# Kernel optimization log

Hardware: AMD Instinct MI355X
Metric: run time of the kernel (lower is better)

## Reference

```python
import jax, jax.numpy as jnp
import numpy as np

L, H, FG, C = 2, 4, 8, 2            # n_layer, grid_heads, grid_feats, grid_channels
HNODE, HNET, HPIN = 96, 32, 16      # hidden node/net/pin feats
ONODE, ONET, NT = 32, 32, 4         # out node/net feats, n_target


def _leaky(x, s=0.01):
    return jnp.where(x >= 0, x, s * x)


def _edge_softmax(e, dst, n):
    # e: [E,H] scores, softmax over incoming edges per dst node
    m = jax.ops.segment_max(e, dst, num_segments=n)
    m = jnp.where(jnp.isfinite(m), m, 0.0)
    ex = jnp.exp(e - m[dst])
    s = jax.ops.segment_sum(ex, dst, num_segments=n)
    return ex / jnp.maximum(s[dst], 1e-9)


def _gat(x, src, dst, fc_w, attn_l, attn_r, bias, n):
    # DGL GATConv: fc (no bias), additive attention, leaky_relu(0.2), edge softmax, sum, +bias
    h = (x @ fc_w).reshape(n, H, FG)                      # [N,H,F]
    el = jnp.sum(h * attn_l, -1)                          # [N,H]
    er = jnp.sum(h * attn_r, -1)
    e = _leaky(el[src] + er[dst], 0.2)                    # [E,H]
    a = _edge_softmax(e, dst, n)
    out = jax.ops.segment_sum(h[src] * a[..., None], dst, num_segments=n)
    return out + bias.reshape(1, H, FG)                   # [N,H,F]


def _graphconv(x, src, dst, w, b, n_src, n_dst):
    # DGL GraphConv norm='both': D_src^-1/2 (xW) aggregated, D_dst^-1/2, + bias
    deg_out = jnp.maximum(jax.ops.segment_sum(jnp.ones(src.shape, jnp.float32), src, num_segments=n_src), 1.0)
    deg_in = jnp.maximum(jax.ops.segment_sum(jnp.ones(dst.shape, jnp.float32), dst, num_segments=n_dst), 1.0)
    h = (x * deg_out[:, None] ** -0.5) @ w
    agg = jax.ops.segment_sum(h[src], dst, num_segments=n_dst)
    return agg * deg_in[:, None] ** -0.5 + b


def _nnconv(x_src, src, dst, efeat, lin2_w, lin2_b, b, n_dst):
    # DGL NNConv (aggregator='mean'): per-edge weight matrix from edge_func=lin2
    W = (efeat @ lin2_w + lin2_b).reshape(-1, HNET, ONODE)   # [E,in,out]
    msg = jnp.einsum('ei,eio->eo', x_src[src], W)            # [E,out]
    deg = jnp.maximum(jax.ops.segment_sum(jnp.ones(dst.shape, jnp.float32), dst, num_segments=n_dst), 1.0)
    agg = jax.ops.segment_sum(msg, dst, num_segments=n_dst) / deg[:, None]
    return agg + b


def setup_inputs() -> dict:
    key = jax.random.key(0)
    ks = jax.random.split(key, 32)
    Nn, Nnet, Ep, Eg = 50000, 50000, 150000, 400000
    IN_NODE, IN_NET, IN_PIN = 16, 8, 8

    def rn(k, shape, scale=0.1):
        return jax.random.normal(k, shape, jnp.float32) * scale

    return {
        'in_node_feat': rn(ks[0], (Nn, IN_NODE), 1.0),
        'in_net_feat': rn(ks[1], (Nnet, IN_NET), 1.0),
        'in_pin_feat': rn(ks[2], (Ep, IN_PIN), 1.0),
        'node_lin_w': rn(ks[3], (IN_NODE, HNODE)), 'node_lin_b': rn(ks[4], (HNODE,)),
        'net_lin_w': rn(ks[5], (IN_NET, HNET)), 'net_lin_b': rn(ks[6], (HNET,)),
        'pin_lin_w': rn(ks[7], (IN_PIN, HPIN)), 'pin_lin_b': rn(ks[8], (HPIN,)),
        'gat_fc_w': rn(ks[9], (L, HNODE, H * FG)),
        'gat_attn_l': rn(ks[10], (L, H, FG)), 'gat_attn_r': rn(ks[11], (L, H, FG)),
        'gat_bias': rn(ks[12], (L, H * FG)),
        'gconv_w': rn(ks[13], (L, HNODE, ONET)), 'gconv_b': rn(ks[14], (L, ONET)),
        'lin2_w': rn(ks[15], (L, HPIN, HNET * ONODE)), 'lin2_b': rn(ks[16], (L, HNET * ONODE)),
        'nnconv_b': rn(ks[17], (L, ONODE)),
        'out1_w': rn(ks[18], (IN_NODE + HNODE, HNODE)), 'out1_b': rn(ks[19], (HNODE,)),
        'out2_w': rn(ks[20], (HNODE, HNODE)), 'out2_b': rn(ks[21], (HNODE,)),
        'out3_w': rn(ks[22], (HNODE, NT)), 'out3_b': rn(ks[23], (NT,)),
        'pins_src': jax.random.randint(ks[24], (Ep,), 0, Nn),
        'pins_dst': jax.random.randint(ks[25], (Ep,), 0, Nnet),
        'grid_src': jax.random.randint(ks[26], (C, Eg), 0, Nn),
        'grid_dst': jax.random.randint(ks[27], (C, Eg), 0, Nn),
    }


def reference(in_node_feat, in_net_feat, in_pin_feat, node_lin_w, node_lin_b,
              net_lin_w, net_lin_b, pin_lin_w, pin_lin_b, gat_fc_w, gat_attn_l,
              gat_attn_r, gat_bias, gconv_w, gconv_b, lin2_w, lin2_b, nnconv_b,
              out1_w, out1_b, out2_w, out2_b, out3_w, out3_b,
              pins_src, pins_dst, grid_src, grid_dst):
    Nn = in_node_feat.shape[0]
    Nnet = in_net_feat.shape[0]
    node = _leaky(in_node_feat @ node_lin_w + node_lin_b)
    net = _leaky(in_net_feat @ net_lin_w + net_lin_b)
    pin = _leaky(in_pin_feat @ pin_lin_w + pin_lin_b)
    for i in range(L):
        grids = [_gat(node, grid_src[j], grid_dst[j], gat_fc_w[i], gat_attn_l[i],
                      gat_attn_r[i], gat_bias[i], Nn) for j in range(C)]
        grid_out = jnp.concatenate(grids, -1).reshape(Nn, -1)   # [N, H*C*FG]
        # 'pins': node -> net (GraphConv); 'pinned': net -> node (NNConv, reversed pin edges)
        net_out = _graphconv(node, pins_src, pins_dst, gconv_w[i], gconv_b[i], Nn, Nnet)
        node_out = _nnconv(net, pins_dst, pins_src, pin, lin2_w[i], lin2_b[i], nnconv_b[i], Nn)
        node = jnp.tanh(jnp.concatenate([grid_out, node_out], -1))
        net = jnp.tanh(net_out)
    h = jnp.tanh(jnp.concatenate([in_node_feat, node], -1) @ out1_w + out1_b)
    h = jnp.tanh(h @ out2_w + out2_b)
    return jax.nn.sigmoid(h @ out3_w + out3_b)
```

## Files before the change

### kernel.cpp

```cpp
#include <hip/hip_runtime.h>
#include <math.h>


#define CAPG 48
#define CAPP 24
#define GB_U16 64
#define PD_U16 32
#define PS_STRIDE 64

typedef unsigned short ushort_t;
typedef unsigned int uint_t;
static __device__ __forceinline__ float bf2f(ushort_t u) {
    return __uint_as_float(((unsigned)u) << 16);
}
static __device__ __forceinline__ ushort_t f2bf(float f) {
    unsigned i = __float_as_uint(f);
    unsigned r = (i + 0x7FFFu + ((i >> 16) & 1u)) >> 16;
    return (ushort_t)r;
}
static __device__ __forceinline__ uint_t pk2(float a, float b) {
    return (uint_t)f2bf(a) | ((uint_t)f2bf(b) << 16);
}
static __device__ __forceinline__ float lo2(uint_t u) { return __uint_as_float(u << 16); }
static __device__ __forceinline__ float hi2(uint_t u) { return __uint_as_float(u & 0xFFFF0000u); }

template <int ACT, int K1, int K2, int M, int R, bool OUT16>
__global__ void gemm_tiled(const float* __restrict__ X1,
                           const float* __restrict__ X2,
                           const float* __restrict__ rowscale,
                           const float* __restrict__ W,
                           const float* __restrict__ bias,
                           void* __restrict__ Yv, int N) {
    constexpr int K = K1 + K2;
    constexpr int MG = M / 4;
    constexpr int RG = 256 / MG;
    __shared__ float sW[K * M];
    for (int t = threadIdx.x; t < K * M; t += 256) sW[t] = W[t];
    __syncthreads();
    const float4* sW4 = (const float4*)sW;
    const int lane = threadIdx.x % MG;
    const int rsub = threadIdx.x / MG;
    if (rsub >= RG) return;
    const long long bstride = (long long)gridDim.x * RG * R;
    for (long long base = (long long)blockIdx.x * RG * R + rsub; base < N; base += bstride) {
        long long rows[R];
        bool ok[R];
        float4 acc[R];
#pragma unroll
        for (int j = 0; j < R; ++j) {
            rows[j] = base + (long long)j * RG;
            ok[j] = rows[j] < N;
            if (!ok[j]) rows[j] = base;
            acc[j] = {0.f, 0.f, 0.f, 0.f};
        }
        {
            const float4* x4[R];
#pragma unroll
            for (int j = 0; j < R; ++j) x4[j] = (const float4*)(X1 + rows[j] * K1);
#pragma unroll 2
            for (int k4 = 0; k4 < K1 / 4; ++k4) {
                float4 w0 = sW4[(k4 * 4 + 0) * MG + lane];
                float4 w1 = sW4[(k4 * 4 + 1) * MG + lane];
                float4 w2 = sW4[(k4 * 4 + 2) * MG + lane];
                float4 w3 = sW4[(k4 * 4 + 3) * MG + lane];
#pragma unroll
                for (int j = 0; j < R; ++j) {
                    float4 xv = x4[j][k4];
                    acc[j].x += xv.x * w0.x + xv.y * w1.x + xv.z * w2.x + xv.w * w3.x;
                    acc[j].y += xv.x * w0.y + xv.y * w1.y + xv.z * w2.y + xv.w * w3.y;
                    acc[j].z += xv.x * w0.z + xv.y * w1.z + xv.z * w2.z + xv.w * w3.z;
                    acc[j].w += xv.x * w0.w + xv.y * w1.w + xv.z * w2.w + xv.w * w3.w;
                }
            }
        }
        if (K2 > 0) {
            const float4* x4[R];
#pragma unroll
            for (int j = 0; j < R; ++j) x4[j] = (const float4*)(X2 + rows[j] * K2);
#pragma unroll 2
            for (int k4 = 0; k4 < K2 / 4; ++k4) {
                float4 w0 = sW4[(K1 + k4 * 4 + 0) * MG + lane];
                float4 w1 = sW4[(K1 + k4 * 4 + 1) * MG + lane];
                float4 w2 = sW4[(K1 + k4 * 4 + 2) * MG + lane];
                float4 w3 = sW4[(K1 + k4 * 4 + 3) * MG + lane];
#pragma unroll
                for (int j = 0; j < R; ++j) {
                    float4 xv = x4[j][k4];
                    acc[j].x += xv.x * w0.x + xv.y * w1.x + xv.z * w2.x + xv.w * w3.x;
                    acc[j].y += xv.x * w0.y + xv.y * w1.y + xv.z * w2.y + xv.w * w3.y;
                    acc[j].z += xv.x * w0.z + xv.y * w1.z + xv.z * w2.z + xv.w * w3.z;
                    acc[j].w += xv.x * w0.w + xv.y * w1.w + xv.z * w2.w + xv.w * w3.w;
                }
            }
        }
#pragma unroll
        for (int j = 0; j < R; ++j) {
            if (!ok[j]) continue;
            float4 a = acc[j];
            if (rowscale) {
                float rs = rowscale[rows[j]];
                a.x *= rs; a.y *= rs; a.z *= rs; a.w *= rs;
            }
            if (bias) {
                float4 bv = *(const float4*)(bias + lane * 4);
                a.x += bv.x; a.y += bv.y; a.z += bv.z; a.w += bv.w;
            }
            if (ACT == 1) {
                a.x = a.x >= 0.f ? a.x : 0.01f * a.x;
                a.y = a.y >= 0.f ? a.y : 0.01f * a.y;
                a.z = a.z >= 0.f ? a.z : 0.01f * a.z;
                a.w = a.w >= 0.f ? a.w : 0.01f * a.w;
            } else if (ACT == 2) {
                a.x = tanhf(a.x); a.y = tanhf(a.y);
                a.z = tanhf(a.z); a.w = tanhf(a.w);
            } else if (ACT == 3) {
                a.x = 1.f / (1.f + expf(-a.x)); a.y = 1.f / (1.f + expf(-a.y));
                a.z = 1.f / (1.f + expf(-a.z)); a.w = 1.f / (1.f + expf(-a.w));
            }
            if (OUT16) {
                uint2 v;
                v.x = pk2(a.x, a.y);
                v.y = pk2(a.z, a.w);
                *(uint2*)((ushort_t*)Yv + rows[j] * M + lane * 4) = v;
            } else {
                *(float4*)((float*)Yv + rows[j] * M + lane * 4) = a;
            }
        }
    }
}

__global__ void gemm_dual32(const float* __restrict__ X,
                            const float* __restrict__ rsN,
                            const float* __restrict__ W1,
                            const float* __restrict__ W2,
                            ushort_t* __restrict__ Y1, ushort_t* __restrict__ Y2, int N) {
    __shared__ float sW1[96 * 32];
    __shared__ float sW2[96 * 32];
    for (int t = threadIdx.x; t < 96 * 32; t += 256) {
        sW1[t] = W1[t];
        sW2[t] = W2[t];
    }
    __syncthreads();
    const float4* sW1_4 = (const float4*)sW1;
    const float4* sW2_4 = (const float4*)sW2;
    const int lane = threadIdx.x & 7;
    const int rsub = threadIdx.x >> 3;
    long long n0 = (long long)blockIdx.x * 64 + rsub;
    long long n1 = n0 + 32;
    if (n0 >= N) return;
    bool ok1 = n1 < N;
    const float4* x0 = (const float4*)(X + n0 * 96);
    const float4* x1 = (const float4*)(X + (ok1 ? n1 : n0) * 96);
    float4 a0 = {0.f, 0.f, 0.f, 0.f}, b0 = a0, a1 = a0, b1 = a0;
#pragma unroll 2
    for (int k4 = 0; k4 < 24; ++k4) {
        float4 xv0 = x0[k4];
        float4 xv1 = x1[k4];
#pragma unroll
        for (int kk = 0; kk < 4; ++kk) {
            float4 w1v = sW1_4[(k4 * 4 + kk) * 8 + lane];
            float4 w2v = sW2_4[(k4 * 4 + kk) * 8 + lane];
            float xs0 = kk == 0 ? xv0.x : kk == 1 ? xv0.y : kk == 2 ? xv0.z : xv0.w;
            float xs1 = kk == 0 ? xv1.x : kk == 1 ? xv1.y : kk == 2 ? xv1.z : xv1.w;
            a0.x += xs0 * w1v.x; a0.y += xs0 * w1v.y; a0.z += xs0 * w1v.z; a0.w += xs0 * w1v.w;
            b0.x += xs0 * w2v.x; b0.y += xs0 * w2v.y; b0.z += xs0 * w2v.z; b0.w += xs0 * w2v.w;
            a1.x += xs1 * w1v.x; a1.y += xs1 * w1v.y; a1.z += xs1 * w1v.z; a1.w += xs1 * w1v.w;
            b1.x += xs1 * w2v.x; b1.y += xs1 * w2v.y; b1.z += xs1 * w2v.z; b1.w += xs1 * w2v.w;
        }
    }
    {
        float rs = rsN[n0];
        uint2 va = {pk2(a0.x, a0.y), pk2(a0.z, a0.w)};
        uint2 vb = {pk2(b0.x * rs, b0.y * rs), pk2(b0.z * rs, b0.w * rs)};
        *(uint2*)(Y1 + n0 * 32 + lane * 4) = va;
        *(uint2*)(Y2 + n0 * 32 + lane * 4) = vb;
    }
    if (ok1) {
        float rs = rsN[n1];
        uint2 va = {pk2(a1.x, a1.y), pk2(a1.z, a1.w)};
        uint2 vb = {pk2(b1.x * rs, b1.y * rs), pk2(b1.z * rs, b1.w * rs)};
        *(uint2*)(Y1 + n1 * 32 + lane * 4) = va;
        *(uint2*)(Y2 + n1 * 32 + lane * 4) = vb;
    }
}

__global__ void zero_counts(ushort_t* __restrict__ gB0, ushort_t* __restrict__ gB1,
                            ushort_t* __restrict__ pdB, int* __restrict__ psB,
                            int Nn, int Nnet) {
    int i = blockIdx.x * blockDim.x + threadIdx.x;
    int mx = Nn > Nnet ? Nn : Nnet;
    for (; i < mx; i += gridDim.x * blockDim.x) {
        if (i < Nn) {
            *(int*)(gB0 + (long long)i * GB_U16) = 0;
            *(int*)(gB1 + (long long)i * GB_U16) = 0;
            psB[(long long)i * PS_STRIDE] = 0;
        }
        if (i < Nnet) *(int*)(pdB + (long long)i * PD_U16) = 0;
    }
}

__global__ void csr_build(const int* __restrict__ ps, const int* __restrict__ pd,
                          const int* __restrict__ gs0, const int* __restrict__ gd0,
                          const int* __restrict__ gs1, const int* __restrict__ gd1,
                          ushort_t* __restrict__ gB0, ushort_t* __restrict__ gB1,
                          ushort_t* __restrict__ pdB, int* __restrict__ psB,
                          int Ep, int Eg) {
    int total = 2 * Ep + 2 * Eg;
    for (int t = blockIdx.x * blockDim.x + threadIdx.x; t < total; t += gridDim.x * blockDim.x) {
        if (t < Ep) {
            int s = ps[t];
            int* b = psB + (long long)s * PS_STRIDE;
            int r = atomicAdd(b, 1);
            if (r < CAPP) ((int2*)b)[1 + r] = make_int2(t, pd[t]);
        } else if (t < 2 * Ep) {
            int e = t - Ep;
            int d = pd[e];
            ushort_t* b = pdB + (long long)d * PD_U16;
            int r = atomicAdd((int*)b, 1);
            if (r < CAPP) b[2 + r] = (ushort_t)ps[e];
        } else if (t < 2 * Ep + Eg) {
            int e = t - 2 * Ep;
            int d = gd0[e];
            ushort_t* b = gB0 + (long long)d * GB_U16;
            int r = atomicAdd((int*)b, 1);
            if (r < CAPG) b[2 + r] = (ushort_t)gs0[e];
        } else {
            int e = t - 2 * Ep - Eg;
            int d = gd1[e];
            ushort_t* b = gB1 + (long long)d * GB_U16;
            int r = atomicAdd((int*)b, 1);
            if (r < CAPG) b[2 + r] = (ushort_t)gs1[e];
        }
    }
}

__global__ void deg_xform2(const int* __restrict__ psB, const ushort_t* __restrict__ pdB,
                           float* __restrict__ rs, float* __restrict__ inv,
                           float* __restrict__ rsNet, int Nn, int Nnet) {
    int i = blockIdx.x * blockDim.x + threadIdx.x;
    int mx = Nn > Nnet ? Nn : Nnet;
    for (; i < mx; i += gridDim.x * blockDim.x) {
        if (i < Nn) {
            float d = fmaxf((float)psB[(long long)i * PS_STRIDE], 1.f);
            rs[i] = 1.f / sqrtf(d);
            inv[i] = 1.f / d;
        }
        if (i < Nnet) {
            float d = fmaxf((float)*(const int*)(pdB + (long long)i * PD_U16), 1.f);
            rsNet[i] = 1.f / sqrtf(d);
        }
    }
}

__global__ void gat_scores(const ushort_t* __restrict__ h, const float* __restrict__ al,
                           const float* __restrict__ ar, float* __restrict__ el,
                           float* __restrict__ er, int N) {
    int idx = blockIdx.x * blockDim.x + threadIdx.x;
    if (idx >= N * 4) return;
    int n = idx >> 2, hd = idx & 3;
    uint4 hv = *(const uint4*)(h + (long long)n * 32 + hd * 8);
    float f0 = lo2(hv.x), f1 = hi2(hv.x), f2 = lo2(hv.y), f3 = hi2(hv.y);
    float f4 = lo2(hv.z), f5 = hi2(hv.z), f6 = lo2(hv.w), f7 = hi2(hv.w);
    const float* a = al + hd * 8;
    const float* r = ar + hd * 8;
    float sl = f0 * a[0] + f1 * a[1] + f2 * a[2] + f3 * a[3] +
               f4 * a[4] + f5 * a[5] + f6 * a[6] + f7 * a[7];
    float sr = f0 * r[0] + f1 * r[1] + f2 * r[2] + f3 * r[3] +
               f4 * r[4] + f5 * r[5] + f6 * r[6] + f7 * r[7];
    el[idx] = sl;
    er[idx] = sr;
}

__global__ void gat_gather8(const ushort_t* __restrict__ gB0, const ushort_t* __restrict__ gB1,
                            const float* __restrict__ el, const float* __restrict__ er,
                            const ushort_t* __restrict__ gh, const float* __restrict__ gbias,
                            float* __restrict__ out, int N) {
    int idx = blockIdx.x * blockDim.x + threadIdx.x;
    if (idx >= N * 8) return;
    int d = idx >> 3;
    int rem = idx & 7;
    int hd = rem >> 1;
    int ch = rem & 1;
    float rd = er[d * 4 + hd];
    const ushort_t* b = (ch ? gB1 : gB0) + (long long)d * GB_U16;
    int c = *(const int*)b;
    c = c < CAPG ? c : CAPG;
    float sum = 0.f;
    float acc0 = 0.f, acc1 = 0.f, acc2 = 0.f, acc3 = 0.f;
    float acc4 = 0.f, acc5 = 0.f, acc6 = 0.f, acc7 = 0.f;
    for (int p = 0; p < c; ++p) {
        int s = b[2 + p];
        float v = el[s * 4 + hd] + rd;
        v = v >= 0.f ? v : 0.2f * v;
        float w = __expf(v);
        uint4 hv = *(const uint4*)(gh + (long long)s * 32 + hd * 8);
        sum += w;
        acc0 += w * lo2(hv.x); acc1 += w * hi2(hv.x);
        acc2 += w * lo2(hv.y); acc3 += w * hi2(hv.y);
        acc4 += w * lo2(hv.z); acc5 += w * hi2(hv.z);
        acc6 += w * lo2(hv.w); acc7 += w * hi2(hv.w);
    }
    float inv = 1.f / fmaxf(sum, 1e-9f);
    const float4* gb4 = (const float4*)(gbias + hd * 8);
    float4 b0 = gb4[0], b1 = gb4[1];
    float* op = out + (long long)d * 96 + hd * 16 + ch * 8;
    float4 r0, r1;
    r0.x = tanhf(acc0 * inv + b0.x); r0.y = tanhf(acc1 * inv + b0.y);
    r0.z = tanhf(acc2 * inv + b0.z); r0.w = tanhf(acc3 * inv + b0.w);
    r1.x = tanhf(acc4 * inv + b1.x); r1.y = tanhf(acc5 * inv + b1.y);
    r1.z = tanhf(acc6 * inv + b1.z); r1.w = tanhf(acc7 * inv + b1.w);
    *(float4*)(op) = r0;
    *(float4*)(op + 4) = r1;
}

__global__ void gconv_gather(const ushort_t* __restrict__ pdB, const ushort_t* __restrict__ h,
                             const float* __restrict__ rsNet, const float* __restrict__ gb,
                             ushort_t* __restrict__ out, int N) {
    long long total = (long long)N * 32;
    long long stride = (long long)gridDim.x * blockDim.x;
    for (long long idx = (long long)blockIdx.x * blockDim.x + threadIdx.x; idx < total; idx += stride) {
        int n = (int)(idx >> 5), c = (int)(idx & 31);
        const ushort_t* b = pdB + (long long)n * PD_U16;
        int cn = *(const int*)b;
        cn = cn < CAPP ? cn : CAPP;
        float acc = 0.f;
        for (int p = 0; p < cn; ++p) acc += bf2f(h[(long long)b[2 + p] * 32 + c]);
        out[idx] = f2bf(tanhf(acc * rsNet[n] + gb[c]));
    }
}

__global__ void nn_accum(const int* __restrict__ psB, const float* __restrict__ pinf,
                         const ushort_t* __restrict__ net, ushort_t* __restrict__ G, int N) {
    int t = blockIdx.x * blockDim.x + threadIdx.x;
    int n = t >> 5, i = t & 31;
    if (n >= N) return;
    const int* b = psB + (long long)n * PS_STRIDE;
    int cn = b[0]; cn = cn < CAPP ? cn : CAPP;
    const int2* ed2 = (const int2*)b + 1;
    float g[17];
#pragma unroll
    for (int k = 0; k < 17; ++k) g[k] = 0.f;
    for (int p = 0; p < cn; ++p) {
        int2 ed = ed2[p];
        float nv = bf2f(net[(long long)ed.y * 32 + i]);
        const float4* pr4 = (const float4*)(pinf + (long long)ed.x * 16);
        float4 a0 = pr4[0], a1 = pr4[1], a2 = pr4[2], a3 = pr4[3];
        g[0] += a0.x * nv;  g[1] += a0.y * nv;  g[2] += a0.z * nv;  g[3] += a0.w * nv;
        g[4] += a1.x * nv;  g[5] += a1.y * nv;  g[6] += a1.z * nv;  g[7] += a1.w * nv;
        g[8] += a2.x * nv;  g[9] += a2.y * nv;  g[10] += a2.z * nv; g[11] += a2.w * nv;
        g[12] += a3.x * nv; g[13] += a3.y * nv; g[14] += a3.z * nv; g[15] += a3.w * nv;
        g[16] += nv;
    }
    ushort_t* Gp = G + (long long)n * 544 + i;
#pragma unroll
    for (int k = 0; k < 17; ++k) Gp[k * 32] = f2bf(g[k]);
}

__launch_bounds__(256, 4)
__global__ void nn_gemm_split(const ushort_t* __restrict__ G, const float* __restrict__ w,
                              const float* __restrict__ b2, float* __restrict__ pA,
                              float* __restrict__ pB, int N) {
    __shared__ float sW[272 * 32];
    const int half = blockIdx.y;
    for (int t = threadIdx.x; t < 272 * 32; t += 256) {
        int grow = half * 272 + (t >> 5);
        int col = t & 31;
        sW[t] = (grow < 512) ? w[grow * 32 + col] : b2[(grow - 512) * 32 + col];
    }
    __syncthreads();
    const float4* sW4 = (const float4*)sW;
    const int lane = threadIdx.x & 7;
    const int rsub = threadIdx.x >> 3;
    long long n0 = (long long)blockIdx.x * 64 + rsub;
    long long n1 = n0 + 32;
    if (n0 >= N) return;
    bool ok1 = n1 < N;
    const ushort4* g0 = (const ushort4*)(G + n0 * 544 + half * 272);
    const ushort4* g1 = (const ushort4*)(G + (ok1 ? n1 : n0) * 544 + half * 272);
    float4 a0 = {0.f, 0.f, 0.f, 0.f}, a1 = {0.f, 0.f, 0.f, 0.f};
#pragma unroll 4
    for (int k4 = 0; k4 < 68; ++k4) {
        float4 w0 = sW4[(k4 * 4 + 0) * 8 + lane];
        float4 w1 = sW4[(k4 * 4 + 1) * 8 + lane];
        float4 w2 = sW4[(k4 * 4 + 2) * 8 + lane];
        float4 w3 = sW4[(k4 * 4 + 3) * 8 + lane];
        ushort4 u0 = g0[k4];
        ushort4 u1 = g1[k4];
        float x0x = bf2f(u0.x), x0y = bf2f(u0.y), x0z = bf2f(u0.z), x0w = bf2f(u0.w);
        float x1x = bf2f(u1.x), x1y = bf2f(u1.y), x1z = bf2f(u1.z), x1w = bf2f(u1.w);
        a0.x += x0x * w0.x + x0y * w1.x + x0z * w2.x + x0w * w3.x;
        a0.y += x0x * w0.y + x0y * w1.y + x0z * w2.y + x0w * w3.y;
        a0.z += x0x * w0.z + x0y * w1.z + x0z * w2.z + x0w * w3.z;
        a0.w += x0x * w0.w + x0y * w1.w + x0z * w2.w + x0w * w3.w;
        a1.x += x1x * w0.x + x1y * w1.x + x1z * w2.x + x1w * w3.x;
        a1.y += x1x * w0.y + x1y * w1.y + x1z * w2.y + x1w * w3.y;
        a1.z += x1x * w0.z + x1y * w1.z + x1z * w2.z + x1w * w3.z;
        a1.w += x1x * w0.w + x1y * w1.w + x1z * w2.w + x1w * w3.w;
    }
    float* dst = half ? pB : pA;
    *(float4*)(dst + n0 * 32 + lane * 4) = a0;
    if (ok1) *(float4*)(dst + n1 * 32 + lane * 4) = a1;
}

__global__ void nn_combine(const float* __restrict__ pA, const float* __restrict__ pB,
                           const float* __restrict__ invN, const float* __restrict__ nnb,
                           float* __restrict__ out, int N) {
    int idx = blockIdx.x * blockDim.x + threadIdx.x;
    if (idx >= N * 8) return;
    int n = idx >> 3, c4 = idx & 7;
    float4 a = ((const float4*)pA)[idx];
    float4 b = ((const float4*)pB)[idx];
    float s = invN[n];
    float4 bv = ((const float4*)nnb)[c4];
    float4 r;
    r.x = tanhf((a.x + b.x) * s + bv.x);
    r.y = tanhf((a.y + b.y) * s + bv.y);
    r.z = tanhf((a.z + b.z) * s + bv.z);
    r.w = tanhf((a.w + b.w) * s + bv.w);
    *(float4*)(out + (long long)n * 96 + 64 + c4 * 4) = r;
}

extern "C" void kernel_launch(void* const* d_in, const int* in_sizes, int n_in,
                              void* d_out, int out_size, void* d_ws, size_t ws_size,
                              hipStream_t stream) {
    const float* in_node = (const float*)d_in[0];
    const float* in_net = (const float*)d_in[1];
    const float* in_pinf = (const float*)d_in[2];
    const float* node_lin_w = (const float*)d_in[3];
    const float* node_lin_b = (const float*)d_in[4];
    const float* net_lin_w = (const float*)d_in[5];
    const float* net_lin_b = (const float*)d_in[6];
    const float* pin_lin_w = (const float*)d_in[7];
    const float* pin_lin_b = (const float*)d_in[8];
    const float* gat_fc_w = (const float*)d_in[9];
    const float* gat_attn_l = (const float*)d_in[10];
    const float* gat_attn_r = (const float*)d_in[11];
    const float* gat_bias = (const float*)d_in[12];
    const float* gconv_w = (const float*)d_in[13];
    const float* gconv_b = (const float*)d_in[14];
    const float* lin2_w = (const float*)d_in[15];
    const float* lin2_b = (const float*)d_in[16];
    const float* nnconv_bias = (const float*)d_in[17];
    const float* out1_w = (const float*)d_in[18];
    const float* out1_b = (const float*)d_in[19];
    const float* out2_w = (const float*)d_in[20];
    const float* out2_b = (const float*)d_in[21];
    const float* out3_w = (const float*)d_in[22];
    const float* out3_b = (const float*)d_in[23];
    const int* pins_src = (const int*)d_in[24];
    const int* pins_dst = (const int*)d_in[25];
    const int* grid_src = (const int*)d_in[26];
    const int* grid_dst = (const int*)d_in[27];

    const int Nn = in_sizes[0] / 16;
    const int Nnet = in_sizes[1] / 8;
    const int Ep = in_sizes[2] / 8;
    const int Eg = in_sizes[26] / 2;

    char* base = (char*)d_ws;
    size_t off = 0;
    auto alloc = [&](size_t bytes) -> void* {
        void* p = base + off;
        off += (bytes + 255) & ~(size_t)255;
        return p;
    };
    float* pin = (float*)alloc((size_t)Ep * 16 * 4);
    ushort_t* G = (ushort_t*)alloc((size_t)Nn * 544 * 2);
    float* pA = (float*)alloc((size_t)Nn * 32 * 4);
    float* pB = (float*)alloc((size_t)Nn * 32 * 4);
    float* rsN = (float*)alloc((size_t)Nn * 4);
    float* invN = (float*)alloc((size_t)Nn * 4);
    float* rsNet = (float*)alloc((size_t)Nnet * 4);
    ushort_t* gridB0 = (ushort_t*)alloc((size_t)Nn * GB_U16 * 2);
    ushort_t* gridB1 = (ushort_t*)alloc((size_t)Nn * GB_U16 * 2);
    ushort_t* pinDstB = (ushort_t*)alloc((size_t)Nnet * PD_U16 * 2);
    int* pinSrcB = (int*)alloc((size_t)Nn * PS_STRIDE * 4);
    float* nodeA = (float*)alloc((size_t)Nn * 96 * 4);
    float* nodeB = (float*)alloc((size_t)Nn * 96 * 4);
    ushort_t* netA = (ushort_t*)alloc((size_t)Nnet * 32 * 2);
    ushort_t* netB = (ushort_t*)alloc((size_t)Nnet * 32 * 2);
    ushort_t* gat_h = (ushort_t*)alloc((size_t)Nn * 32 * 2);
    float* el = (float*)alloc((size_t)Nn * 4 * 4);
    float* er = (float*)alloc((size_t)Nn * 4 * 4);
    ushort_t* gconv_h = (ushort_t*)alloc((size_t)Nn * 32 * 2);

    auto gsz = [](long long total) -> int {
        long long b = (total + 255) / 256;
        if (b < 1) b = 1;
        if (b > 4096) b = 4096;
        return (int)b;
    };

    const int maxN = Nn > Nnet ? Nn : Nnet;
    const long long scatterT = 2LL * Ep + 2LL * Eg;

    zero_counts<<<gsz(maxN), 256, 0, stream>>>(gridB0, gridB1, pinDstB, pinSrcB, Nn, Nnet);
    csr_build<<<gsz(scatterT), 256, 0, stream>>>(pins_src, pins_dst,
                                                 grid_src, grid_dst, grid_src + Eg, grid_dst + Eg,
                                                 gridB0, gridB1, pinDstB, pinSrcB, Ep, Eg);
    deg_xform2<<<gsz(maxN), 256, 0, stream>>>(pinSrcB, pinDstB, rsN, invN, rsNet, Nn, Nnet);

    auto blocks_for = [](long long N, int M, int R) -> int {
        int rowsPerBlock = (256 / (M / 4)) * R;
        long long b = (N + rowsPerBlock - 1) / rowsPerBlock;
        if (b > 2048) b = 2048;
        if (b < 1) b = 1;
        return (int)b;
    };

    gemm_tiled<1, 16, 0, 96, 4, false><<<blocks_for(Nn, 96, 4), 256, 0, stream>>>(
        in_node, nullptr, nullptr, node_lin_w, node_lin_b, nodeA, Nn);
    gemm_tiled<1, 8, 0, 32, 2, true><<<blocks_for(Nnet, 32, 2), 256, 0, stream>>>(
        in_net, nullptr, nullptr, net_lin_w, net_lin_b, netA, Nnet);
    gemm_tiled<1, 8, 0, 16, 2, false><<<blocks_for(Ep, 16, 2), 256, 0, stream>>>(
        in_pinf, nullptr, nullptr, pin_lin_w, pin_lin_b, pin, Ep);

    float* node_cur = nodeA; float* node_nxt = nodeB;
    ushort_t* net_cur = netA; ushort_t* net_nxt = netB;

    for (int i = 0; i < 2; ++i) {
        gemm_dual32<<<(Nn + 63) / 64, 256, 0, stream>>>(
            node_cur, rsN, gat_fc_w + (size_t)i * 96 * 32, gconv_w + (size_t)i * 96 * 32,
            gat_h, gconv_h, Nn);
        gat_scores<<<(Nn * 4 + 255) / 256, 256, 0, stream>>>(
            gat_h, gat_attn_l + i * 32, gat_attn_r + i * 32, el, er, Nn);

        gat_gather8<<<(Nn * 8 + 255) / 256, 256, 0, stream>>>(
            gridB0, gridB1, el, er, gat_h, gat_bias + i * 32, node_nxt, Nn);

        gconv_gather<<<gsz((long long)Nnet * 32), 256, 0, stream>>>(
            pinDstB, gconv_h, rsNet, gconv_b + i * 32, net_nxt, Nnet);

        nn_accum<<<(Nn * 32 + 255) / 256, 256, 0, stream>>>(
            pinSrcB, pin, net_cur, G, Nn);
        {
            dim3 g((Nn + 63) / 64, 2);
            nn_gemm_split<<<g, 256, 0, stream>>>(
                G, lin2_w + (size_t)i * 16 * 1024, lin2_b + (size_t)i * 1024, pA, pB, Nn);
        }
        nn_combine<<<(Nn * 8 + 255) / 256, 256, 0, stream>>>(
            pA, pB, invN, nnconv_bias + i * 32, node_nxt, Nn);

        float* t = node_cur; node_cur = node_nxt; node_nxt = t;
        ushort_t* u = net_cur; net_cur = net_nxt; net_nxt = u;
    }

    float* h1 = node_nxt;
    gemm_tiled<2, 16, 96, 96, 4, false><<<blocks_for(Nn, 96, 4), 256, 0, stream>>>(
        in_node, node_cur, nullptr, out1_w, out1_b, h1, Nn);
    float* h2 = node_cur;
    gemm_tiled<2, 96, 0, 96, 4, false><<<blocks_for(Nn, 96, 4), 256, 0, stream>>>(
        h1, nullptr, nullptr, out2_w, out2_b, h2, Nn);
    gemm_tiled<3, 96, 0, 4, 1, false><<<blocks_for(Nn, 4, 1), 256, 0, stream>>>(
        h2, nullptr, nullptr, out3_w, out3_b, (float*)d_out, Nn);
}
```

Baseline: 400.8 us.

## Use bf16 MFMA for NNConv GEMM and fuse mean/bias/tanh epilogue

Replaces the scalar FP32 split-K NNConv GEMM and its separate combine kernel with a single kernel using 16x16x32 bf16 MFMA instructions. The weights are converted to bf16 and pre-swizzled in shared memory, and the mean normalisation, bias and tanh are applied in the epilogue. This removes the pA/pB partial buffers and one kernel launch, and moves the matmul onto matrix cores. The cost is bf16 rounding of the weights and a larger per-block weight staging step.

```diff
diff --git a/kernel.cpp b/kernel.cpp
--- a/kernel.cpp
+++ b/kernel.cpp
@@ -10,6 +10,9 @@
 
 typedef unsigned short ushort_t;
 typedef unsigned int uint_t;
+typedef __attribute__((ext_vector_type(8))) short bf16x8;
+typedef __attribute__((ext_vector_type(4))) float f32x4;
+
 static __device__ __forceinline__ float bf2f(ushort_t u) {
     return __uint_as_float(((unsigned)u) << 16);
 }
@@ -357,67 +360,54 @@
 }
 
 __launch_bounds__(256, 4)
-__global__ void nn_gemm_split(const ushort_t* __restrict__ G, const float* __restrict__ w,
-                              const float* __restrict__ b2, float* __restrict__ pA,
-                              float* __restrict__ pB, int N) {
-    __shared__ float sW[272 * 32];
-    const int half = blockIdx.y;
-    for (int t = threadIdx.x; t < 272 * 32; t += 256) {
-        int grow = half * 272 + (t >> 5);
-        int col = t & 31;
-        sW[t] = (grow < 512) ? w[grow * 32 + col] : b2[(grow - 512) * 32 + col];
+__global__ void nn_gemm_mfma(const ushort_t* __restrict__ G,
+                             const float* __restrict__ w,
+                             const float* __restrict__ b2,
+                             const float* __restrict__ invN,
+                             const float* __restrict__ nnb,
+                             float* __restrict__ out, int N) {
+    __shared__ ushort_t sB[2 * 17 * 64 * 8];
+    for (int idx = threadIdx.x; idx < 2 * 17 * 64 * 8; idx += 256) {
+        int e = idx & 7;
+        int l = (idx >> 3) & 63;
+        int rest = idx >> 9;
+        int s = rest % 17;
+        int t = rest / 17;
+        int grow = s * 32 + ((l >> 4) << 3) + e;
+        int col = t * 16 + (l & 15);
+        float v = (grow < 512) ? w[grow * 32 + col] : b2[(grow - 512) * 32 + col];
+        sB[idx] = f2bf(v);
     }
     __syncthreads();
-    const float4* sW4 = (const float4*)sW;
-    const int lane = threadIdx.x & 7;
-    const int rsub = threadIdx.x >> 3;
-    long long n0 = (long long)blockIdx.x * 64 + rsub;
-    long long n1 = n0 + 32;
-    if (n0 >= N) return;
-    bool ok1 = n1 < N;
-    const ushort4* g0 = (const ushort4*)(G + n0 * 544 + half * 272);
-    const ushort4* g1 = (const ushort4*)(G + (ok1 ? n1 : n0) * 544 + half * 272);
-    float4 a0 = {0.f, 0.f, 0.f, 0.f}, a1 = {0.f, 0.f, 0.f, 0.f};
-#pragma unroll 4
-    for (int k4 = 0; k4 < 68; ++k4) {
-        float4 w0 = sW4[(k4 * 4 + 0) * 8 + lane];
-        float4 w1 = sW4[(k4 * 4 + 1) * 8 + lane];
-        float4 w2 = sW4[(k4 * 4 + 2) * 8 + lane];
-        float4 w3 = sW4[(k4 * 4 + 3) * 8 + lane];
-        ushort4 u0 = g0[k4];
-        ushort4 u1 = g1[k4];
-        float x0x = bf2f(u0.x), x0y = bf2f(u0.y), x0z = bf2f(u0.z), x0w = bf2f(u0.w);
-        float x1x = bf2f(u1.x), x1y = bf2f(u1.y), x1z = bf2f(u1.z), x1w = bf2f(u1.w);
-        a0.x += x0x * w0.x + x0y * w1.x + x0z * w2.x + x0w * w3.x;
-        a0.y += x0x * w0.y + x0y * w1.y + x0z * w2.y + x0w * w3.y;
-        a0.z += x0x * w0.z + x0y * w1.z + x0z * w2.z + x0w * w3.z;
-        a0.w += x0x * w0.w + x0y * w1.w + x0z * w2.w + x0w * w3.w;
-        a1.x += x1x * w0.x + x1y * w1.x + x1z * w2.x + x1w * w3.x;
-        a1.y += x1x * w0.y + x1y * w1.y + x1z * w2.y + x1w * w3.y;
-        a1.z += x1x * w0.z + x1y * w1.z + x1z * w2.z + x1w * w3.z;
-        a1.w += x1x * w0.w + x1y * w1.w + x1z * w2.w + x1w * w3.w;
-    }
-    float* dst = half ? pB : pA;
-    *(float4*)(dst + n0 * 32 + lane * 4) = a0;
-    if (ok1) *(float4*)(dst + n1 * 32 + lane * 4) = a1;
-}
-
-__global__ void nn_combine(const float* __restrict__ pA, const float* __restrict__ pB,
-                           const float* __restrict__ invN, const float* __restrict__ nnb,
-                           float* __restrict__ out, int N) {
-    int idx = blockIdx.x * blockDim.x + threadIdx.x;
-    if (idx >= N * 8) return;
-    int n = idx >> 3, c4 = idx & 7;
-    float4 a = ((const float4*)pA)[idx];
-    float4 b = ((const float4*)pB)[idx];
-    float s = invN[n];
-    float4 bv = ((const float4*)nnb)[c4];
-    float4 r;
-    r.x = tanhf((a.x + b.x) * s + bv.x);
-    r.y = tanhf((a.y + b.y) * s + bv.y);
-    r.z = tanhf((a.z + b.z) * s + bv.z);
-    r.w = tanhf((a.w + b.w) * s + bv.w);
-    *(float4*)(out + (long long)n * 96 + 64 + c4 * 4) = r;
+    const int lane = threadIdx.x & 63;
+    const int wv = threadIdx.x >> 6;
+    long long rowBase = (long long)blockIdx.x * 64 + (long long)wv * 16;
+    if (rowBase >= N) return;
+    const int r15 = lane & 15;
+    const int kgrp = lane >> 4;
+    long long arow = rowBase + r15;
+    if (arow >= N) arow = N - 1;
+    const ushort_t* gp = G + arow * 544 + kgrp * 8;
+    f32x4 acc0 = {0.f, 0.f, 0.f, 0.f};
+    f32x4 acc1 = {0.f, 0.f, 0.f, 0.f};
+#pragma unroll
+    for (int s = 0; s < 17; ++s) {
+        bf16x8 a = *(const bf16x8*)(gp + s * 32);
+        bf16x8 bb0 = *(const bf16x8*)(sB + ((0 * 17 + s) * 64 + lane) * 8);
+        bf16x8 bb1 = *(const bf16x8*)(sB + ((1 * 17 + s) * 64 + lane) * 8);
+        acc0 = __builtin_amdgcn_mfma_f32_16x16x32_bf16(a, bb0, acc0, 0, 0, 0);
+        acc1 = __builtin_amdgcn_mfma_f32_16x16x32_bf16(a, bb1, acc1, 0, 0, 0);
+    }
+#pragma unroll
+    for (int r = 0; r < 4; ++r) {
+        long long row = rowBase + kgrp * 4 + r;
+        if (row < N) {
+            float iv = invN[row];
+            float* op = out + row * 96 + 64;
+            op[r15] = tanhf(acc0[r] * iv + nnb[r15]);
+            op[16 + r15] = tanhf(acc1[r] * iv + nnb[16 + r15]);
+        }
+    }
 }
 
 extern "C" void kernel_launch(void* const* d_in, const int* in_sizes, int n_in,
@@ -466,8 +456,6 @@
     };
     float* pin = (float*)alloc((size_t)Ep * 16 * 4);
     ushort_t* G = (ushort_t*)alloc((size_t)Nn * 544 * 2);
-    float* pA = (float*)alloc((size_t)Nn * 32 * 4);
-    float* pB = (float*)alloc((size_t)Nn * 32 * 4);
     float* rsN = (float*)alloc((size_t)Nn * 4);
     float* invN = (float*)alloc((size_t)Nn * 4);
     float* rsNet = (float*)alloc((size_t)Nnet * 4);
@@ -533,13 +521,9 @@
 
         nn_accum<<<(Nn * 32 + 255) / 256, 256, 0, stream>>>(
             pinSrcB, pin, net_cur, G, Nn);
-        {
-            dim3 g((Nn + 63) / 64, 2);
-            nn_gemm_split<<<g, 256, 0, stream>>>(
-                G, lin2_w + (size_t)i * 16 * 1024, lin2_b + (size_t)i * 1024, pA, pB, Nn);
-        }
-        nn_combine<<<(Nn * 8 + 255) / 256, 256, 0, stream>>>(
-            pA, pB, invN, nnconv_bias + i * 32, node_nxt, Nn);
+        nn_gemm_mfma<<<(Nn + 63) / 64, 256, 0, stream>>>(
+            G, lin2_w + (size_t)i * 16 * 1024, lin2_b + (size_t)i * 1024,
+            invN, nnconv_bias + i * 32, node_nxt, Nn);
 
         float* t = node_cur; node_cur = node_nxt; node_nxt = t;
         ushort_t* u = net_cur; net_cur = net_nxt; net_nxt = u;
```

Result: faster. 361.7 us (-9.8%).
